# Performance work log

Measured on AMD Instinct MI355X. Metric: run time of the kernel, lower is better.

Reference implementation:

```python
import jax, jax.numpy as jnp
import numpy as np

H, W = 256, 256
N = H * W
C0, C1, C2 = 16, 32, 64  # base, base*2, base*4


def _grid_edges(h, w):
    """8-neighborhood grid edges (directed, both directions) + self loops."""
    idx = np.arange(h * w).reshape(h, w)
    srcs, dsts = [], []
    for dy in (-1, 0, 1):
        for dx in (-1, 0, 1):
            if dy == 0 and dx == 0:
                continue
            s = idx[max(0, -dy):h - max(0, dy), max(0, -dx):w - max(0, dx)]
            d = idx[max(0, dy):h - max(0, -dy), max(0, dx):w - max(0, -dx)]
            srcs.append(s.ravel()); dsts.append(d.ravel())
    srcs.append(np.arange(h * w)); dsts.append(np.arange(h * w))  # GATConv add_self_loops
    return np.concatenate(srcs).astype(np.int32), np.concatenate(dsts).astype(np.int32)


def _conv2d(x, w, b, pad):
    y = jax.lax.conv_general_dilated(x, w, (1, 1), [(pad, pad), (pad, pad)],
                                     dimension_numbers=('NCHW', 'OIHW', 'NCHW'))
    return y + b[None, :, None, None]


def _bn(x, g, b, eps=1e-5):
    # training-mode BatchNorm2d: biased batch statistics over (N,H,W)
    mu = x.mean((0, 2, 3), keepdims=True)
    var = ((x - mu) ** 2).mean((0, 2, 3), keepdims=True)
    return g[None, :, None, None] * (x - mu) * jax.lax.rsqrt(var + eps) + b[None, :, None, None]


def _gat(xg, w, a_s, a_d, b, src, dst):
    # PyG GATConv, heads=1: gather -> leaky_relu attention -> softmax over dst -> scatter-add
    def one(xn):
        h = xn @ w.T                                   # [N, C_out]
        e = jax.nn.leaky_relu((h @ a_s)[src] + (h @ a_d)[dst], 0.2)  # [E]
        m = jax.ops.segment_max(e, dst, num_segments=N)
        p = jnp.exp(e - m[dst])
        denom = jax.ops.segment_sum(p, dst, num_segments=N)
        agg = jax.ops.segment_sum(h[src] * p[:, None], dst, num_segments=N)
        return agg / (denom[:, None] + 1e-16) + b
    return jax.vmap(one)(xg)


def _gcb(x, pos_w, pos_b, gw, gas, gad, gb, src, dst):
    B, C = x.shape[0], x.shape[1]
    px = jnp.linspace(-1.0, 1.0, W)
    py = jnp.linspace(-1.0, 1.0, H)
    gx, gy = jnp.meshgrid(px, py, indexing='xy')       # each (H, W)
    pos = jnp.stack([gy, gx], -1)                      # (H, W, 2)
    pe = pos @ pos_w.T + pos_b                         # (H, W, C)
    x = x + pe.transpose(2, 0, 1)[None]
    xg = x.transpose(0, 2, 3, 1).reshape(B, N, C)      # batch of disjoint graphs -> vmap
    out = _gat(xg, gw, gas, gad, gb, src, dst)
    return out.reshape(B, H, W, -1).transpose(0, 3, 1, 2)


def _forward(x, conv1_w, conv1_b, bn1_g, bn1_b,
             pos1_w, pos1_b, gat1_w, gat1_as, gat1_ad, gat1_b, bn2_g, bn2_b,
             pos2_w, pos2_b, gat2_w, gat2_as, gat2_ad, gat2_b, bn3_g, bn3_b,
             mlp1_w, mlp1_b, mlp2_w, mlp2_b, filt, filt_bias,
             enh1_w, enh1_b, enh2_w, enh2_b, bn4_g, bn4_b, src, dst):
    f = _bn(jax.nn.relu(_conv2d(x, conv1_w, conv1_b, 2)), bn1_g, bn1_b)
    f = _bn(jax.nn.relu(_gcb(f, pos1_w, pos1_b, gat1_w, gat1_as, gat1_ad, gat1_b, src, dst)), bn2_g, bn2_b)
    f = _bn(jax.nn.relu(_gcb(f, pos2_w, pos2_b, gat2_w, gat2_as, gat2_ad, gat2_b, src, dst)), bn3_g, bn3_b)
    pooled = f.mean((2, 3))                            # AdaptiveAvgPool2d(1)
    h = jax.nn.relu(pooled @ mlp1_w.T + mlp1_b)
    cw = jax.nn.softmax(h @ mlp2_w.T + mlp2_b, axis=1)[:, :, None, None]
    wf = f * cw
    ff = wf * filt + filt_bias
    enh = _conv2d(jax.nn.relu(_conv2d(ff, enh1_w, enh1_b, 1)), enh2_w, enh2_b, 1) + ff
    return _bn(jax.nn.relu(enh), bn4_g, bn4_b)


def setup_inputs() -> dict:
    key = jax.random.key(0)
    ks = iter(jax.random.split(key, 40))
    def rn(shape, s=0.1):
        return jax.random.normal(next(ks), shape, dtype=jnp.float32) * s
    src, dst = _grid_edges(H, W)
    return {
        'x': jax.random.normal(next(ks), (2, 1, H, W), dtype=jnp.float32),
        'conv1_w': rn((C0, 1, 5, 5)), 'conv1_b': rn((C0,)),
        'bn1_g': jnp.ones((C0,)), 'bn1_b': jnp.zeros((C0,)),
        'pos1_w': rn((C0, 2)), 'pos1_b': rn((C0,)),
        'gat1_w': rn((C1, C0)), 'gat1_as': rn((C1,)), 'gat1_ad': rn((C1,)), 'gat1_b': rn((C1,)),
        'bn2_g': jnp.ones((C1,)), 'bn2_b': jnp.zeros((C1,)),
        'pos2_w': rn((C1, 2)), 'pos2_b': rn((C1,)),
        'gat2_w': rn((C2, C1)), 'gat2_as': rn((C2,)), 'gat2_ad': rn((C2,)), 'gat2_b': rn((C2,)),
        'bn3_g': jnp.ones((C2,)), 'bn3_b': jnp.zeros((C2,)),
        'mlp1_w': rn((C2 // 4, C2)), 'mlp1_b': rn((C2 // 4,)),
        'mlp2_w': rn((C2, C2 // 4)), 'mlp2_b': rn((C2,)),
        'filt': jnp.ones((1, C2, H, W)), 'filt_bias': jnp.zeros((1, C2, 1, 1)),
        'enh1_w': rn((C2 // 2, C2, 3, 3)), 'enh1_b': rn((C2 // 2,)),
        'enh2_w': rn((C2, C2 // 2, 3, 3)), 'enh2_b': rn((C2,)),
        'bn4_g': jnp.ones((C2,)), 'bn4_b': jnp.zeros((C2,)),
        'src': jnp.asarray(src), 'dst': jnp.asarray(dst),
    }


def reference(x, conv1_w, conv1_b, bn1_g, bn1_b,
              pos1_w, pos1_b, gat1_w, gat1_as, gat1_ad, gat1_b, bn2_g, bn2_b,
              pos2_w, pos2_b, gat2_w, gat2_as, gat2_ad, gat2_b, bn3_g, bn3_b,
              mlp1_w, mlp1_b, mlp2_w, mlp2_b, filt, filt_bias,
              enh1_w, enh1_b, enh2_w, enh2_b, bn4_g, bn4_b, src, dst):
    return _forward(x, conv1_w, conv1_b, bn1_g, bn1_b,
                    pos1_w, pos1_b, gat1_w, gat1_as, gat1_ad, gat1_b, bn2_g, bn2_b,
                    pos2_w, pos2_b, gat2_w, gat2_as, gat2_ad, gat2_b, bn3_g, bn3_b,
                    mlp1_w, mlp1_b, mlp2_w, mlp2_b, filt, filt_bias,
                    enh1_w, enh1_b, enh2_w, enh2_b, bn4_g, bn4_b, src, dst)
```

## Files before the change

### kernel.cpp

```cpp
#include <hip/hip_runtime.h>
#include <math.h>

#define HH 256
#define WW 256
#define NPIX 65536
#define BATCH 2

#define OFF_W0   0u
#define OFF_W1   8388608u
#define OFF_W2   16777216u
#define OFF_W3   20971520u
#define OFF_S    25165824u
#define OFF_D    25296896u
#define OFF_STAT 25427968u
#define OFF_ST1  (OFF_STAT + 0u)
#define OFF_ST2  (OFF_STAT + 64u)
#define OFF_ST3  (OFF_STAT + 192u)
#define OFF_ST4  (OFF_STAT + 448u)
#define OFF_CW   (OFF_STAT + 576u)
#define STAT_ZERO_N 704
#define OFF_WB1  (OFF_STAT + 704u)
#define OFF_WB2  (OFF_WB1 + 18432u)

typedef __attribute__((ext_vector_type(8))) short bf8v;
typedef __attribute__((ext_vector_type(4))) float f4v;
typedef __attribute__((ext_vector_type(4))) unsigned short us4;

#define GLL16(g, l) __builtin_amdgcn_global_load_lds(                               \
    (const __attribute__((address_space(1))) unsigned int*)(g),                    \
    (__attribute__((address_space(3))) unsigned int*)(l), 16, 0, 0)

__device__ __forceinline__ unsigned short f2bf(float f) {
    unsigned u = __float_as_uint(f);
    return (unsigned short)((u + 0x7FFFu + ((u >> 16) & 1u)) >> 16);
}
__device__ __forceinline__ float bf2f(unsigned short u) {
    return __uint_as_float(((unsigned)u) << 16);
}

__device__ __forceinline__ void bn_coef(const float* __restrict__ raw,
                                        const float* __restrict__ g,
                                        const float* __restrict__ b,
                                        int C, int c, float& A, float& Bv) {
    const float inv = 1.f / (float)(BATCH * NPIX);
    float mu  = raw[c] * inv;
    float var = raw[C + c] * inv - mu * mu;
    float rinv = rsqrtf(var + 1e-5f);
    A  = g[c] * rinv;
    Bv = b[c] - A * mu;
}

__device__ __forceinline__ void wave_red2(float& s, float& q) {
#pragma unroll
    for (int off = 32; off; off >>= 1) {
        s += __shfl_xor(s, off);
        q += __shfl_xor(q, off);
    }
}

__device__ __forceinline__ void row_swz512(int bid, int& y, int& b) {
    int orig = (bid & 7) * 64 + (bid >> 3);
    y = orig & 255;
    b = orig >> 8;
}

__global__ void prep(float* __restrict__ st,
                     const float* __restrict__ w1, unsigned short* __restrict__ wb1,
                     const float* __restrict__ w2, unsigned short* __restrict__ wb2) {
    int bid = blockIdx.x, tid = threadIdx.x;
    if (bid < 3) {
        int i = bid * 256 + tid;
        if (i < STAT_ZERO_N) st[i] = 0.f;
    } else if (bid < 75) {
        int i = (bid - 3) * 256 + tid;
        int co = i / (64 * 9);
        int rem = i - co * 64 * 9;
        int ci = rem / 9;
        int pos = rem - ci * 9;
        wb1[(pos * 32 + co) * 64 + ci] = f2bf(w1[i]);
    } else {
        int i = (bid - 75) * 256 + tid;
        int co = i / (32 * 9);
        int rem = i - co * 32 * 9;
        int ci = rem / 9;
        int pos = rem - ci * 9;
        wb2[(pos * 64 + co) * 32 + ci] = f2bf(w2[i]);
    }
}

__global__ __launch_bounds__(256) void conv5x5_all(const float* __restrict__ x,
                                                   const float* __restrict__ w,
                                                   const float* __restrict__ bias,
                                                   unsigned short* __restrict__ out,
                                                   float* __restrict__ st) {
    int y = blockIdx.x, b = blockIdx.y;
    int xx = threadIdx.x;
    __shared__ float lds[5 * 260];
    __shared__ float red[2][16][4];
    for (int i = threadIdx.x; i < 5 * 260; i += 256) {
        int r = i / 260, pos = i - r * 260;
        int yy = y + r - 2, xc = pos - 2;
        float v = 0.f;
        if ((unsigned)yy < 256u && (unsigned)xc < 256u) v = x[(b << 16) + (yy << 8) + xc];
        lds[i] = v;
    }
    __syncthreads();
    float v[25];
#pragma unroll
    for (int r = 0; r < 5; r++)
#pragma unroll
        for (int c = 0; c < 5; c++) v[r * 5 + c] = lds[r * 260 + xx + c];
    int lane = threadIdx.x & 63, wv = threadIdx.x >> 6;
#pragma unroll
    for (int co = 0; co < 16; co++) {
        float acc = bias[co];
#pragma unroll
        for (int k = 0; k < 25; k++) acc = fmaf(v[k], w[co * 25 + k], acc);
        acc = fmaxf(acc, 0.f);
        out[((size_t)(b * 16 + co) << 16) + (y << 8) + xx] = f2bf(acc);
        float s = acc, q = acc * acc;
        wave_red2(s, q);
        if (lane == 0) { red[0][co][wv] = s; red[1][co][wv] = q; }
    }
    __syncthreads();
    if (threadIdx.x < 16) {
        int co = threadIdx.x;
        float s = red[0][co][0] + red[0][co][1] + red[0][co][2] + red[0][co][3];
        float q = red[1][co][0] + red[1][co][1] + red[1][co][2] + red[1][co][3];
        atomicAdd(&st[co], s);
        atomicAdd(&st[16 + co], q);
    }
}

template <int CI, int CO>
__global__ void gat_pre(const unsigned short* __restrict__ f, const float* __restrict__ raw,
                        const float* __restrict__ bng, const float* __restrict__ bnb,
                        const float* __restrict__ posw, const float* __restrict__ posb,
                        const float* __restrict__ gw, const float* __restrict__ gas,
                        const float* __restrict__ gad,
                        unsigned short* __restrict__ hout, float* __restrict__ sout,
                        float* __restrict__ dout) {
    int tid = blockIdx.x * 256 + threadIdx.x;
    int n = tid & (NPIX - 1);
    int b = tid >> 16;
    int y = n >> 8, x = n & 255;
    float py = y * (2.f / 255.f) - 1.f;
    float px = x * (2.f / 255.f) - 1.f;
    float v[CI];
#pragma unroll
    for (int ci = 0; ci < CI; ci++) {
        float A, Bv;
        bn_coef(raw, bng, bnb, CI, ci, A, Bv);
        float t = fmaf(bf2f(f[(size_t)(b * CI + ci) * NPIX + n]), A, Bv);
        v[ci] = t + posw[2 * ci] * py + posw[2 * ci + 1] * px + posb[ci];
    }
    float s = 0.f, d = 0.f;
    for (int co = 0; co < CO; co++) {
        float acc = 0.f;
#pragma unroll
        for (int ci = 0; ci < CI; ci++) acc = fmaf(v[ci], gw[co * CI + ci], acc);
        hout[(size_t)(b * CO + co) * NPIX + n] = f2bf(acc);
        s = fmaf(acc, gas[co], s);
        d = fmaf(acc, gad[co], d);
    }
    sout[tid] = s;
    dout[tid] = d;
}

template <int CO, bool POOL>
__global__ __launch_bounds__(256) void gat_stencil_mfma(const unsigned short* __restrict__ hb,
                                                        const float* __restrict__ sbuf,
                                                        const float* __restrict__ dbuf,
                                                        const float* __restrict__ gb,
                                                        unsigned short* __restrict__ out,
                                                        float* __restrict__ st) {
    constexpr int NT2 = CO / 32;
    constexpr int CH = CO / 2;
    int bid = blockIdx.x;
    int orig = (bid & 7) * 128 + (bid >> 3);
    int coh = orig & 1;
    int rowu = orig >> 1;
    int y = rowu & 255;
    int b = rowu >> 8;
    int tid = threadIdx.x, lane = tid & 63, wid = tid >> 6;
    int m = lane & 15, grp = lane >> 4;
    int xw = wid * 64;
    int x = xw + lane;
    float di = dbuf[(b << 16) + (y << 8) + x];
    float p[9], mx = -1e30f;
#pragma unroll
    for (int k = 0; k < 9; k++) {
        int dy = k / 3 - 1, dx = k % 3 - 1;
        int yy = y + dy, xxn = x + dx;
        bool ok = ((unsigned)yy < 256u) && ((unsigned)xxn < 256u);
        float e = -1e30f;
        if (ok) {
            float t = sbuf[(b << 16) + (yy << 8) + xxn] + di;
            e = t > 0.f ? t : 0.2f * t;
        }
        p[k] = e;
        mx = fmaxf(mx, e);
    }
    float den = 0.f;
#pragma unroll
    for (int k = 0; k < 9; k++) { p[k] = __expf(p[k] - mx); den += p[k]; }
    float rden = 1.f / (den + 1e-16f);
    unsigned short pb[9];
#pragma unroll
    for (int k = 0; k < 9; k++) pb[k] = f2bf(p[k] * rden);
    unsigned pk0 = (unsigned)pb[0] | ((unsigned)pb[1] << 16);
    unsigned pk1 = (unsigned)pb[2] | ((unsigned)pb[3] << 16);
    unsigned pk2 = (unsigned)pb[4] | ((unsigned)pb[5] << 16);
    unsigned pk3 = (unsigned)pb[6] | ((unsigned)pb[7] << 16);
    unsigned pk4 = (unsigned)pb[8];
    float sAcc[NT2], qAcc[NT2], bb[NT2];
#pragma unroll
    for (int ct = 0; ct < NT2; ct++) {
        sAcc[ct] = 0.f; qAcc[ct] = 0.f;
        bb[ct] = gb[coh * CH + ct * 16 + m];
    }
#pragma unroll 1
    for (int t = 0; t < 4; t++) {
        int xb = xw + t * 16;
        int src = t * 16 + m;
        unsigned rk0 = __shfl(pk0, src);
        unsigned rk1 = __shfl(pk1, src);
        unsigned rk2 = __shfl(pk2, src);
        unsigned rk3 = __shfl(pk3, src);
        unsigned rk4 = __shfl(pk4, src);
        unsigned short rb[9];
        rb[0] = (unsigned short)rk0; rb[1] = (unsigned short)(rk0 >> 16);
        rb[2] = (unsigned short)rk1; rb[3] = (unsigned short)(rk1 >> 16);
        rb[4] = (unsigned short)rk2; rb[5] = (unsigned short)(rk2 >> 16);
        rb[6] = (unsigned short)rk3; rb[7] = (unsigned short)(rk3 >> 16);
        rb[8] = (unsigned short)rk4;
        union { bf8v v; unsigned short h[8]; } af[3];
#pragma unroll
        for (int dyi = 0; dyi < 3; dyi++)
#pragma unroll
            for (int j = 0; j < 8; j++) {
                int k = grp * 8 + j;
                int d = k - 8 - m;
                af[dyi].h[j] = (d >= -1 && d <= 1) ? rb[dyi * 3 + d + 1] : (unsigned short)0;
            }
        f4v acc[NT2];
        f4v z4 = {0.f, 0.f, 0.f, 0.f};
#pragma unroll
        for (int ct = 0; ct < NT2; ct++) acc[ct] = z4;
        int px0 = xb - 8 + grp * 8;
        px0 = px0 < 0 ? 0 : (px0 > 248 ? 248 : px0);
#pragma unroll
        for (int dyi = 0; dyi < 3; dyi++) {
            int yy = y + dyi - 1;
            if ((unsigned)yy >= 256u) continue;
#pragma unroll
            for (int ct = 0; ct < NT2; ct++) {
                int ch = coh * CH + ct * 16 + m;
                bf8v bv = *(const bf8v*)(hb + (((size_t)(b * CO + ch)) << 16) + (yy << 8) + px0);
                acc[ct] = __builtin_amdgcn_mfma_f32_16x16x32_bf16(af[dyi].v, bv, acc[ct], 0, 0, 0);
            }
        }
        int pxr = xb + grp * 4;
#pragma unroll
        for (int ct = 0; ct < NT2; ct++) {
            int ch = coh * CH + ct * 16 + m;
            f4v a = acc[ct];
            float o0 = fmaxf(a[0] + bb[ct], 0.f);
            float o1 = fmaxf(a[1] + bb[ct], 0.f);
            float o2 = fmaxf(a[2] + bb[ct], 0.f);
            float o3 = fmaxf(a[3] + bb[ct], 0.f);
            us4 pkst = {f2bf(o0), f2bf(o1), f2bf(o2), f2bf(o3)};
            *(us4*)(out + (((size_t)(b * CO + ch)) << 16) + (y << 8) + pxr) = pkst;
            sAcc[ct] += o0 + o1 + o2 + o3;
            qAcc[ct] += o0 * o0 + o1 * o1 + o2 * o2 + o3 * o3;
        }
    }
#pragma unroll
    for (int ct = 0; ct < NT2; ct++) {
        sAcc[ct] += __shfl_xor(sAcc[ct], 16); sAcc[ct] += __shfl_xor(sAcc[ct], 32);
        qAcc[ct] += __shfl_xor(qAcc[ct], 16); qAcc[ct] += __shfl_xor(qAcc[ct], 32);
    }
    __shared__ float red[2][NT2][16][4];
    if (grp == 0) {
#pragma unroll
        for (int ct = 0; ct < NT2; ct++) {
            red[0][ct][m][wid] = sAcc[ct];
            red[1][ct][m][wid] = qAcc[ct];
        }
    }
    __syncthreads();
    if (tid < CH) {
        int ct = tid >> 4, mm = tid & 15;
        int c = coh * CH + tid;
        float s = red[0][ct][mm][0] + red[0][ct][mm][1] + red[0][ct][mm][2] + red[0][ct][mm][3];
        float qq = red[1][ct][mm][0] + red[1][ct][mm][1] + red[1][ct][mm][2] + red[1][ct][mm][3];
        atomicAdd(&st[c], s);
        atomicAdd(&st[CO + c], qq);
        if (POOL) atomicAdd(&st[2 * CO + b * CO + c], s);
    }
}

__global__ void mlp_cw(const float* __restrict__ raw3, const float* __restrict__ g3,
                       const float* __restrict__ b3, const float* __restrict__ w1,
                       const float* __restrict__ bb1, const float* __restrict__ w2,
                       const float* __restrict__ bb2, float* __restrict__ cw) {
    __shared__ float pooled[2][64];
    __shared__ float hsh[2][16];
    int tid = threadIdx.x;
    {
        int b = tid >> 6, c = tid & 63;
        float A, Bv;
        bn_coef(raw3, g3, b3, 64, c, A, Bv);
        float sm = raw3[128 + (b << 6) + c];
        pooled[b][c] = fmaf(sm * (1.f / 65536.f), A, Bv);
    }
    __syncthreads();
    if (tid < 32) {
        int b = tid >> 4, j = tid & 15;
        float acc = bb1[j];
        for (int c2 = 0; c2 < 64; c2++) acc = fmaf(pooled[b][c2], w1[(j << 6) + c2], acc);
        hsh[b][j] = fmaxf(acc, 0.f);
    }
    __syncthreads();
    int b = tid >> 6, c = tid & 63;
    float logit = bb2[c];
    for (int j = 0; j < 16; j++) logit = fmaf(hsh[b][j], w2[(c << 4) + j], logit);
    float mm = logit;
#pragma unroll
    for (int off = 32; off; off >>= 1) mm = fmaxf(mm, __shfl_xor(mm, off));
    float e = __expf(logit - mm);
    float ss = e;
#pragma unroll
    for (int off = 32; off; off >>= 1) ss += __shfl_xor(ss, off);
    cw[(b << 6) + c] = e / ss;
}

__global__ __launch_bounds__(256) void ff_t(const unsigned short* __restrict__ g64,
                                            const float* __restrict__ raw3,
                                            const float* __restrict__ g3,
                                            const float* __restrict__ b3,
                                            const float* __restrict__ cw,
                                            const float* __restrict__ filt,
                                            const float* __restrict__ fbias,
                                            unsigned short* __restrict__ ffout,
                                            unsigned* __restrict__ at1) {
    int pxb = blockIdx.x * 64;
    int b = pxb >> 16;
    int nb = pxb & 65535;
    __shared__ unsigned t[64 * 33];
    int tid = threadIdx.x;
#pragma unroll
    for (int k = 0; k < 2; k++) {
        int u = tid + k * 256;
        int q = u & 15;
        int cp = u >> 4;
        int ch0 = cp * 2, ch1 = ch0 + 1;
        float A0, B0, A1, B1;
        bn_coef(raw3, g3, b3, 64, ch0, A0, B0);
        bn_coef(raw3, g3, b3, 64, ch1, A1, B1);
        float s0 = cw[(b << 6) + ch0], s1 = cw[(b << 6) + ch1];
        float fb0 = fbias[ch0], fb1 = fbias[ch1];
        int n = nb + q * 4;
        us4 r0 = *(const us4*)(g64 + ((size_t)(b * 64 + ch0) << 16) + n);
        us4 r1 = *(const us4*)(g64 + ((size_t)(b * 64 + ch1) << 16) + n);
        float4 l0 = *(const float4*)(filt + ((size_t)ch0 << 16) + n);
        float4 l1 = *(const float4*)(filt + ((size_t)ch1 << 16) + n);
        float4 o0, o1;
        o0.x = fmaf(fmaf(bf2f(r0[0]), A0, B0) * s0, l0.x, fb0);
        o0.y = fmaf(fmaf(bf2f(r0[1]), A0, B0) * s0, l0.y, fb0);
        o0.z = fmaf(fmaf(bf2f(r0[2]), A0, B0) * s0, l0.z, fb0);
        o0.w = fmaf(fmaf(bf2f(r0[3]), A0, B0) * s0, l0.w, fb0);
        o1.x = fmaf(fmaf(bf2f(r1[0]), A1, B1) * s1, l1.x, fb1);
        o1.y = fmaf(fmaf(bf2f(r1[1]), A1, B1) * s1, l1.y, fb1);
        o1.z = fmaf(fmaf(bf2f(r1[2]), A1, B1) * s1, l1.z, fb1);
        o1.w = fmaf(fmaf(bf2f(r1[3]), A1, B1) * s1, l1.w, fb1);
        us4 f0 = {f2bf(o0.x), f2bf(o0.y), f2bf(o0.z), f2bf(o0.w)};
        us4 f1 = {f2bf(o1.x), f2bf(o1.y), f2bf(o1.z), f2bf(o1.w)};
        *(us4*)(ffout + ((size_t)(b * 64 + ch0) << 16) + n) = f0;
        *(us4*)(ffout + ((size_t)(b * 64 + ch1) << 16) + n) = f1;
#pragma unroll
        for (int i = 0; i < 4; i++)
            t[(q * 4 + i) * 33 + cp] = (unsigned)f0[i] | ((unsigned)f1[i] << 16);
    }
    __syncthreads();
#pragma unroll
    for (int j = 0; j < 8; j++) {
        int lin = j * 256 + tid;
        int pl = lin >> 5, cp = lin & 31;
        unsigned v = t[pl * 33 + cp];
        int P = pxb + pl;
        size_t byte = ((size_t)P << 7) + ((cp >= 16) ? 64 : 0)
                    + (((cp & 15) * 4) ^ (((P >> 1) & 3) << 4));
        *(unsigned*)((char*)at1 + byte) = v;
    }
}

__global__ __launch_bounds__(256) void enh1_mfma(const unsigned short* __restrict__ at1,
                                                 const unsigned short* __restrict__ wb,
                                                 const float* __restrict__ bias,
                                                 unsigned short* __restrict__ at2) {
    int y, b;
    row_swz512(blockIdx.x, y, b);
    int tid = threadIdx.x;
    int lane = tid & 63, wid = tid >> 6;
    __shared__ __align__(16) unsigned short lds_u16[3 * 258 * 32];
    char* ldsb = (char*)lds_u16;
    {
        bf8v z = {0, 0, 0, 0, 0, 0, 0, 0};
        for (int i = tid; i < 3 * 258 * 32 / 8; i += 256) ((bf8v*)lds_u16)[i] = z;
    }
    f4v acc[4][2];
    {
        f4v z4 = {0.f, 0.f, 0.f, 0.f};
#pragma unroll
        for (int m = 0; m < 4; m++) { acc[m][0] = z4; acc[m][1] = z4; }
    }
#pragma unroll 1
    for (int kh = 0; kh < 2; kh++) {
        __syncthreads();
        for (int c = wid; c < 48; c += 4) {
            int r = c >> 4, k = c & 15;
            int yy = y + r - 1;
            if ((unsigned)yy < 256u) {
                const char* src = (const char*)at1
                    + (((size_t)((b << 16) + (yy << 8)) + (k * 16 + (lane >> 2))) << 7)
                    + kh * 64 + (lane & 3) * 16;
                char* dst = ldsb + (r * 258 + 1) * 64 + k * 1024;
                GLL16(src, dst);
            }
        }
        __syncthreads();
        bf8v bw0[9], bw1[9];
#pragma unroll
        for (int pos = 0; pos < 9; pos++) {
            bw0[pos] = *(const bf8v*)(wb + (pos * 32 + (lane & 15)) * 64 + kh * 32 + (lane >> 4) * 8);
            bw1[pos] = *(const bf8v*)(wb + (pos * 32 + 16 + (lane & 15)) * 64 + kh * 32 + (lane >> 4) * 8);
        }
#pragma unroll
        for (int mt = 0; mt < 4; mt++) {
            int xb = (wid * 4 + mt) * 16 + (lane & 15);
#pragma unroll
            for (int ky = 0; ky < 3; ky++) {
#pragma unroll
                for (int kx = 0; kx < 3; kx++) {
                    int x = xb + kx - 1;
                    int s = x + 1;
                    int off = (ky * 258 + s) * 64 + (((lane >> 4) * 16) ^ (((x >> 1) & 3) << 4));
                    bf8v a = *(const bf8v*)(ldsb + off);
                    acc[mt][0] = __builtin_amdgcn_mfma_f32_16x16x32_bf16(a, bw0[ky * 3 + kx], acc[mt][0], 0, 0, 0);
                    acc[mt][1] = __builtin_amdgcn_mfma_f32_16x16x32_bf16(a, bw1[ky * 3 + kx], acc[mt][1], 0, 0, 0);
                }
            }
        }
    }
    float bb[2] = {bias[lane & 15], bias[16 + (lane & 15)]};
#pragma unroll
    for (int mt = 0; mt < 4; mt++) {
#pragma unroll
        for (int nt = 0; nt < 2; nt++) {
            f4v v = acc[mt][nt];
            int co = nt * 16 + (lane & 15);
#pragma unroll
            for (int r = 0; r < 4; r++) {
                int x = (wid * 4 + mt) * 16 + (lane >> 4) * 4 + r;
                float val = fmaxf(v[r] + bb[nt], 0.f);
                size_t byte = (((size_t)((b << 16) + (y << 8) + x)) << 6)
                            + ((co * 2) ^ (((x >> 1) & 3) << 4));
                *(unsigned short*)((char*)at2 + byte) = f2bf(val);
            }
        }
    }
}

__global__ __launch_bounds__(256) void enh2_mfma(const unsigned short* __restrict__ at2,
                                                 const unsigned short* __restrict__ wb,
                                                 const float* __restrict__ bias,
                                                 const unsigned short* __restrict__ ff,
                                                 float* __restrict__ out,
                                                 float* __restrict__ st) {
    int y, b;
    row_swz512(blockIdx.x, y, b);
    int tid = threadIdx.x;
    int lane = tid & 63, wid = tid >> 6;
    __shared__ __align__(16) unsigned short lds_u16[3 * 258 * 32];
    char* ldsb = (char*)lds_u16;
    {
        bf8v z = {0, 0, 0, 0, 0, 0, 0, 0};
        for (int i = tid; i < 3 * 258 * 32 / 8; i += 256) ((bf8v*)lds_u16)[i] = z;
    }
    __syncthreads();
    for (int c = wid; c < 48; c += 4) {
        int r = c >> 4, k = c & 15;
        int yy = y + r - 1;
        if ((unsigned)yy < 256u) {
            const char* src = (const char*)at2
                + (((size_t)((b << 16) + (yy << 8))) << 6) + k * 1024 + lane * 16;
            char* dst = ldsb + (r * 258 + 1) * 64 + k * 1024;
            GLL16(src, dst);
        }
    }
    __syncthreads();
    f4v acc[4][4];
    {
        f4v z4 = {0.f, 0.f, 0.f, 0.f};
#pragma unroll
        for (int m = 0; m < 4; m++)
#pragma unroll
            for (int n = 0; n < 4; n++) acc[m][n] = z4;
    }
#pragma unroll
    for (int np = 0; np < 2; np++) {
        bf8v bw0[9], bw1[9];
#pragma unroll
        for (int pos = 0; pos < 9; pos++) {
            bw0[pos] = *(const bf8v*)(wb + (pos * 64 + np * 32 + (lane & 15)) * 32 + (lane >> 4) * 8);
            bw1[pos] = *(const bf8v*)(wb + (pos * 64 + np * 32 + 16 + (lane & 15)) * 32 + (lane >> 4) * 8);
        }
#pragma unroll
        for (int mt = 0; mt < 4; mt++) {
            int xb = (wid * 4 + mt) * 16 + (lane & 15);
#pragma unroll
            for (int ky = 0; ky < 3; ky++) {
#pragma unroll
                for (int kx = 0; kx < 3; kx++) {
                    int x = xb + kx - 1;
                    int s = x + 1;
                    int off = (ky * 258 + s) * 64 + (((lane >> 4) * 16) ^ (((x >> 1) & 3) << 4));
                    bf8v a = *(const bf8v*)(ldsb + off);
                    acc[mt][2 * np]     = __builtin_amdgcn_mfma_f32_16x16x32_bf16(a, bw0[ky * 3 + kx], acc[mt][2 * np], 0, 0, 0);
                    acc[mt][2 * np + 1] = __builtin_amdgcn_mfma_f32_16x16x32_bf16(a, bw1[ky * 3 + kx], acc[mt][2 * np + 1], 0, 0, 0);
                }
            }
        }
    }
    __syncthreads();
    float* red = (float*)lds_u16;
#pragma unroll
    for (int nt = 0; nt < 4; nt++) {
        int co = nt * 16 + (lane & 15);
        float bb = bias[co];
        float s = 0.f, q = 0.f;
#pragma unroll
        for (int mt = 0; mt < 4; mt++) {
            int xb4 = (wid * 4 + mt) * 16 + (lane >> 4) * 4;
            size_t idx = ((size_t)(b * 64 + co) << 16) + (y << 8) + xb4;
            us4 rv = *(const us4*)(ff + idx);
            f4v a = acc[mt][nt];
            float4 o;
            o.x = fmaxf(a[0] + bb + bf2f(rv[0]), 0.f);
            o.y = fmaxf(a[1] + bb + bf2f(rv[1]), 0.f);
            o.z = fmaxf(a[2] + bb + bf2f(rv[2]), 0.f);
            o.w = fmaxf(a[3] + bb + bf2f(rv[3]), 0.f);
            *(float4*)(out + idx) = o;
            s += o.x + o.y + o.z + o.w;
            q += o.x * o.x + o.y * o.y + o.z * o.z + o.w * o.w;
        }
        s += __shfl_xor(s, 16); s += __shfl_xor(s, 32);
        q += __shfl_xor(q, 16); q += __shfl_xor(q, 32);
        if (lane < 16) {
            red[(co * 4 + wid) * 2 + 0] = s;
            red[(co * 4 + wid) * 2 + 1] = q;
        }
    }
    __syncthreads();
    if (tid < 64) {
        float s = 0.f, q = 0.f;
#pragma unroll
        for (int w = 0; w < 4; w++) {
            s += red[(tid * 4 + w) * 2 + 0];
            q += red[(tid * 4 + w) * 2 + 1];
        }
        atomicAdd(&st[tid], s);
        atomicAdd(&st[64 + tid], q);
    }
}

__global__ void bn_apply4(float4* __restrict__ io, const float* __restrict__ raw,
                          const float* __restrict__ g, const float* __restrict__ b) {
    int t = blockIdx.x * 256 + threadIdx.x;
    int c = (t >> 14) & 63;
    float A, Bv;
    bn_coef(raw, g, b, 64, c, A, Bv);
    float4 v = io[t];
    v.x = fmaf(v.x, A, Bv);
    v.y = fmaf(v.y, A, Bv);
    v.z = fmaf(v.z, A, Bv);
    v.w = fmaf(v.w, A, Bv);
    io[t] = v;
}

extern "C" void kernel_launch(void* const* d_in, const int* in_sizes, int n_in,
                              void* d_out, int out_size, void* d_ws, size_t ws_size,
                              hipStream_t stream) {
    const float* x       = (const float*)d_in[0];
    const float* conv1_w = (const float*)d_in[1];
    const float* conv1_b = (const float*)d_in[2];
    const float* bn1_g   = (const float*)d_in[3];
    const float* bn1_b   = (const float*)d_in[4];
    const float* pos1_w  = (const float*)d_in[5];
    const float* pos1_b  = (const float*)d_in[6];
    const float* gat1_w  = (const float*)d_in[7];
    const float* gat1_as = (const float*)d_in[8];
    const float* gat1_ad = (const float*)d_in[9];
    const float* gat1_b  = (const float*)d_in[10];
    const float* bn2_g   = (const float*)d_in[11];
    const float* bn2_b   = (const float*)d_in[12];
    const float* pos2_w  = (const float*)d_in[13];
    const float* pos2_b  = (const float*)d_in[14];
    const float* gat2_w  = (const float*)d_in[15];
    const float* gat2_as = (const float*)d_in[16];
    const float* gat2_ad = (const float*)d_in[17];
    const float* gat2_b  = (const float*)d_in[18];
    const float* bn3_g   = (const float*)d_in[19];
    const float* bn3_b   = (const float*)d_in[20];
    const float* mlp1_w  = (const float*)d_in[21];
    const float* mlp1_b  = (const float*)d_in[22];
    const float* mlp2_w  = (const float*)d_in[23];
    const float* mlp2_b  = (const float*)d_in[24];
    const float* filt    = (const float*)d_in[25];
    const float* fbias   = (const float*)d_in[26];
    const float* enh1_w  = (const float*)d_in[27];
    const float* enh1_b  = (const float*)d_in[28];
    const float* enh2_w  = (const float*)d_in[29];
    const float* enh2_b  = (const float*)d_in[30];
    const float* bn4_g   = (const float*)d_in[31];
    const float* bn4_b   = (const float*)d_in[32];

    float* ws = (float*)d_ws;
    unsigned short* P0 = (unsigned short*)(ws + OFF_W0);
    unsigned short* HB = (unsigned short*)(ws + OFF_W1);
    unsigned short* FFB = (unsigned short*)(ws + OFF_W1);
    unsigned* AT1 = (unsigned*)(ws + OFF_W2);
    unsigned short* AT2 = (unsigned short*)(ws + OFF_W3);
    float* SB = ws + OFF_S;
    float* DB = ws + OFF_D;
    float* ST1 = ws + OFF_ST1;
    float* ST2 = ws + OFF_ST2;
    float* ST3 = ws + OFF_ST3;
    float* ST4 = ws + OFF_ST4;
    float* CW  = ws + OFF_CW;
    unsigned short* WB1 = (unsigned short*)(ws + OFF_WB1);
    unsigned short* WB2 = (unsigned short*)(ws + OFF_WB2);
    float* out = (float*)d_out;

    prep<<<147, 256, 0, stream>>>(ws + OFF_STAT, enh1_w, WB1, enh2_w, WB2);

    conv5x5_all<<<dim3(256, 2), 256, 0, stream>>>(x, conv1_w, conv1_b, P0, ST1);

    gat_pre<16, 32><<<512, 256, 0, stream>>>(P0, ST1, bn1_g, bn1_b, pos1_w, pos1_b,
                                             gat1_w, gat1_as, gat1_ad, HB, SB, DB);

    gat_stencil_mfma<32, false><<<1024, 256, 0, stream>>>(HB, SB, DB, gat1_b, P0, ST2);

    gat_pre<32, 64><<<512, 256, 0, stream>>>(P0, ST2, bn2_g, bn2_b, pos2_w, pos2_b,
                                             gat2_w, gat2_as, gat2_ad, HB, SB, DB);

    gat_stencil_mfma<64, true><<<1024, 256, 0, stream>>>(HB, SB, DB, gat2_b, P0, ST3);

    mlp_cw<<<1, 128, 0, stream>>>(ST3, bn3_g, bn3_b, mlp1_w, mlp1_b, mlp2_w, mlp2_b, CW);

    ff_t<<<2048, 256, 0, stream>>>(P0, ST3, bn3_g, bn3_b, CW, filt, fbias, FFB, AT1);

    enh1_mfma<<<512, 256, 0, stream>>>((const unsigned short*)AT1, WB1, enh1_b, AT2);

    enh2_mfma<<<512, 256, 0, stream>>>(AT2, WB2, enh2_b, FFB, out, ST4);

    bn_apply4<<<32768 / 4, 256, 0, stream>>>((float4*)out, ST4, bn4_g, bn4_b);
}
```

Before: 189.4 us.

## Fuse channel-weight MLP into ff_t, stage enh2 output in bf16, hoist BN coefs

The single-block mlp_cw kernel is removed and every ff_t block now recomputes the pooled MLP and softmax channel weights into shared memory, saving a launch and a serialization point at the cost of redundant per-block work. enh2 now writes its pre-BN result as bf16 to a workspace buffer instead of fp32 to the output, and bn_apply4 reads the bf16 data and writes fp32, which cuts the intermediate read/write traffic but loses precision before normalization. gat_pre computes BN coefficients once per block in shared memory instead of per thread per channel.

```diff
diff --git a/kernel.cpp b/kernel.cpp
--- a/kernel.cpp
+++ b/kernel.cpp
@@ -17,7 +17,6 @@
 #define OFF_ST2  (OFF_STAT + 64u)
 #define OFF_ST3  (OFF_STAT + 192u)
 #define OFF_ST4  (OFF_STAT + 448u)
-#define OFF_CW   (OFF_STAT + 576u)
 #define STAT_ZERO_N 704
 #define OFF_WB1  (OFF_STAT + 704u)
 #define OFF_WB2  (OFF_WB1 + 18432u)
@@ -133,13 +132,22 @@
 }
 
 template <int CI, int CO>
-__global__ void gat_pre(const unsigned short* __restrict__ f, const float* __restrict__ raw,
+__global__ __launch_bounds__(256) void gat_pre(const unsigned short* __restrict__ f,
+                        const float* __restrict__ raw,
                         const float* __restrict__ bng, const float* __restrict__ bnb,
                         const float* __restrict__ posw, const float* __restrict__ posb,
                         const float* __restrict__ gw, const float* __restrict__ gas,
                         const float* __restrict__ gad,
                         unsigned short* __restrict__ hout, float* __restrict__ sout,
                         float* __restrict__ dout) {
+    __shared__ float Ash[CI], Bsh[CI];
+    if (threadIdx.x < CI) {
+        float A, Bv;
+        bn_coef(raw, bng, bnb, CI, threadIdx.x, A, Bv);
+        Ash[threadIdx.x] = A;
+        Bsh[threadIdx.x] = Bv + posb[threadIdx.x];
+    }
+    __syncthreads();
     int tid = blockIdx.x * 256 + threadIdx.x;
     int n = tid & (NPIX - 1);
     int b = tid >> 16;
@@ -149,10 +157,8 @@
     float v[CI];
 #pragma unroll
     for (int ci = 0; ci < CI; ci++) {
-        float A, Bv;
-        bn_coef(raw, bng, bnb, CI, ci, A, Bv);
-        float t = fmaf(bf2f(f[(size_t)(b * CI + ci) * NPIX + n]), A, Bv);
-        v[ci] = t + posw[2 * ci] * py + posw[2 * ci + 1] * px + posb[ci];
+        float t = fmaf(bf2f(f[(size_t)(b * CI + ci) * NPIX + n]), Ash[ci], Bsh[ci]);
+        v[ci] = t + posw[2 * ci] * py + posw[2 * ci + 1] * px;
     }
     float s = 0.f, d = 0.f;
     for (int co = 0; co < CO; co++) {
@@ -300,14 +306,24 @@
     }
 }
 
-__global__ void mlp_cw(const float* __restrict__ raw3, const float* __restrict__ g3,
-                       const float* __restrict__ b3, const float* __restrict__ w1,
-                       const float* __restrict__ bb1, const float* __restrict__ w2,
-                       const float* __restrict__ bb2, float* __restrict__ cw) {
+__global__ __launch_bounds__(256) void ff_t(const unsigned short* __restrict__ g64,
+                                            const float* __restrict__ raw3,
+                                            const float* __restrict__ g3,
+                                            const float* __restrict__ b3,
+                                            const float* __restrict__ w1,
+                                            const float* __restrict__ bb1,
+                                            const float* __restrict__ w2,
+                                            const float* __restrict__ bb2,
+                                            const float* __restrict__ filt,
+                                            const float* __restrict__ fbias,
+                                            unsigned short* __restrict__ ffout,
+                                            unsigned* __restrict__ at1) {
     __shared__ float pooled[2][64];
     __shared__ float hsh[2][16];
+    __shared__ float cwsh[2][64];
+    __shared__ unsigned t[64 * 33];
     int tid = threadIdx.x;
-    {
+    if (tid < 128) {
         int b = tid >> 6, c = tid & 63;
         float A, Bv;
         bn_coef(raw3, g3, b3, 64, c, A, Bv);
@@ -322,33 +338,23 @@
         hsh[b][j] = fmaxf(acc, 0.f);
     }
     __syncthreads();
-    int b = tid >> 6, c = tid & 63;
-    float logit = bb2[c];
-    for (int j = 0; j < 16; j++) logit = fmaf(hsh[b][j], w2[(c << 4) + j], logit);
-    float mm = logit;
-#pragma unroll
-    for (int off = 32; off; off >>= 1) mm = fmaxf(mm, __shfl_xor(mm, off));
-    float e = __expf(logit - mm);
-    float ss = e;
-#pragma unroll
-    for (int off = 32; off; off >>= 1) ss += __shfl_xor(ss, off);
-    cw[(b << 6) + c] = e / ss;
-}
-
-__global__ __launch_bounds__(256) void ff_t(const unsigned short* __restrict__ g64,
-                                            const float* __restrict__ raw3,
-                                            const float* __restrict__ g3,
-                                            const float* __restrict__ b3,
-                                            const float* __restrict__ cw,
-                                            const float* __restrict__ filt,
-                                            const float* __restrict__ fbias,
-                                            unsigned short* __restrict__ ffout,
-                                            unsigned* __restrict__ at1) {
+    if (tid < 128) {
+        int b = tid >> 6, c = tid & 63;
+        float logit = bb2[c];
+        for (int j = 0; j < 16; j++) logit = fmaf(hsh[b][j], w2[(c << 4) + j], logit);
+        float mm = logit;
+#pragma unroll
+        for (int off = 32; off; off >>= 1) mm = fmaxf(mm, __shfl_xor(mm, off));
+        float e = __expf(logit - mm);
+        float ss = e;
+#pragma unroll
+        for (int off = 32; off; off >>= 1) ss += __shfl_xor(ss, off);
+        cwsh[b][c] = e / ss;
+    }
+    __syncthreads();
     int pxb = blockIdx.x * 64;
     int b = pxb >> 16;
     int nb = pxb & 65535;
-    __shared__ unsigned t[64 * 33];
-    int tid = threadIdx.x;
 #pragma unroll
     for (int k = 0; k < 2; k++) {
         int u = tid + k * 256;
@@ -358,7 +364,7 @@
         float A0, B0, A1, B1;
         bn_coef(raw3, g3, b3, 64, ch0, A0, B0);
         bn_coef(raw3, g3, b3, 64, ch1, A1, B1);
-        float s0 = cw[(b << 6) + ch0], s1 = cw[(b << 6) + ch1];
+        float s0 = cwsh[b][ch0], s1 = cwsh[b][ch1];
         float fb0 = fbias[ch0], fb1 = fbias[ch1];
         int n = nb + q * 4;
         us4 r0 = *(const us4*)(g64 + ((size_t)(b * 64 + ch0) << 16) + n);
@@ -476,7 +482,7 @@
                                                  const unsigned short* __restrict__ wb,
                                                  const float* __restrict__ bias,
                                                  const unsigned short* __restrict__ ff,
-                                                 float* __restrict__ out,
+                                                 unsigned short* __restrict__ enh,
                                                  float* __restrict__ st) {
     int y, b;
     row_swz512(blockIdx.x, y, b);
@@ -546,14 +552,15 @@
             size_t idx = ((size_t)(b * 64 + co) << 16) + (y << 8) + xb4;
             us4 rv = *(const us4*)(ff + idx);
             f4v a = acc[mt][nt];
-            float4 o;
-            o.x = fmaxf(a[0] + bb + bf2f(rv[0]), 0.f);
-            o.y = fmaxf(a[1] + bb + bf2f(rv[1]), 0.f);
-            o.z = fmaxf(a[2] + bb + bf2f(rv[2]), 0.f);
-            o.w = fmaxf(a[3] + bb + bf2f(rv[3]), 0.f);
-            *(float4*)(out + idx) = o;
-            s += o.x + o.y + o.z + o.w;
-            q += o.x * o.x + o.y * o.y + o.z * o.z + o.w * o.w;
+            us4 ro;
+            ro[0] = f2bf(fmaxf(a[0] + bb + bf2f(rv[0]), 0.f));
+            ro[1] = f2bf(fmaxf(a[1] + bb + bf2f(rv[1]), 0.f));
+            ro[2] = f2bf(fmaxf(a[2] + bb + bf2f(rv[2]), 0.f));
+            ro[3] = f2bf(fmaxf(a[3] + bb + bf2f(rv[3]), 0.f));
+            *(us4*)(enh + idx) = ro;
+            float r0 = bf2f(ro[0]), r1 = bf2f(ro[1]), r2 = bf2f(ro[2]), r3 = bf2f(ro[3]);
+            s += r0 + r1 + r2 + r3;
+            q += r0 * r0 + r1 * r1 + r2 * r2 + r3 * r3;
         }
         s += __shfl_xor(s, 16); s += __shfl_xor(s, 32);
         q += __shfl_xor(q, 16); q += __shfl_xor(q, 32);
@@ -575,18 +582,20 @@
     }
 }
 
-__global__ void bn_apply4(float4* __restrict__ io, const float* __restrict__ raw,
+__global__ void bn_apply4(const us4* __restrict__ enh, float4* __restrict__ io,
+                          const float* __restrict__ raw,
                           const float* __restrict__ g, const float* __restrict__ b) {
     int t = blockIdx.x * 256 + threadIdx.x;
     int c = (t >> 14) & 63;
     float A, Bv;
     bn_coef(raw, g, b, 64, c, A, Bv);
-    float4 v = io[t];
-    v.x = fmaf(v.x, A, Bv);
-    v.y = fmaf(v.y, A, Bv);
-    v.z = fmaf(v.z, A, Bv);
-    v.w = fmaf(v.w, A, Bv);
-    io[t] = v;
+    us4 v = enh[t];
+    float4 o;
+    o.x = fmaf(bf2f(v[0]), A, Bv);
+    o.y = fmaf(bf2f(v[1]), A, Bv);
+    o.z = fmaf(bf2f(v[2]), A, Bv);
+    o.w = fmaf(bf2f(v[3]), A, Bv);
+    io[t] = o;
 }
 
 extern "C" void kernel_launch(void* const* d_in, const int* in_sizes, int n_in,
@@ -631,6 +640,7 @@
     unsigned short* HB = (unsigned short*)(ws + OFF_W1);
     unsigned short* FFB = (unsigned short*)(ws + OFF_W1);
     unsigned* AT1 = (unsigned*)(ws + OFF_W2);
+    unsigned short* ENH = (unsigned short*)(ws + OFF_W2);
     unsigned short* AT2 = (unsigned short*)(ws + OFF_W3);
     float* SB = ws + OFF_S;
     float* DB = ws + OFF_D;
@@ -638,7 +648,6 @@
     float* ST2 = ws + OFF_ST2;
     float* ST3 = ws + OFF_ST3;
     float* ST4 = ws + OFF_ST4;
-    float* CW  = ws + OFF_CW;
     unsigned short* WB1 = (unsigned short*)(ws + OFF_WB1);
     unsigned short* WB2 = (unsigned short*)(ws + OFF_WB2);
     float* out = (float*)d_out;
@@ -657,13 +666,12 @@
 
     gat_stencil_mfma<64, true><<<1024, 256, 0, stream>>>(HB, SB, DB, gat2_b, P0, ST3);
 
-    mlp_cw<<<1, 128, 0, stream>>>(ST3, bn3_g, bn3_b, mlp1_w, mlp1_b, mlp2_w, mlp2_b, CW);
-
-    ff_t<<<2048, 256, 0, stream>>>(P0, ST3, bn3_g, bn3_b, CW, filt, fbias, FFB, AT1);
+    ff_t<<<2048, 256, 0, stream>>>(P0, ST3, bn3_g, bn3_b, mlp1_w, mlp1_b, mlp2_w, mlp2_b,
+                                   filt, fbias, FFB, AT1);
 
     enh1_mfma<<<512, 256, 0, stream>>>((const unsigned short*)AT1, WB1, enh1_b, AT2);
 
-    enh2_mfma<<<512, 256, 0, stream>>>(AT2, WB2, enh2_b, FFB, out, ST4);
-
-    bn_apply4<<<32768 / 4, 256, 0, stream>>>((float4*)out, ST4, bn4_g, bn4_b);
-}
+    enh2_mfma<<<512, 256, 0, stream>>>(AT2, WB2, enh2_b, FFB, ENH, ST4);
+
+    bn_apply4<<<8192, 256, 0, stream>>>((const us4*)ENH, (float4*)out, ST4, bn4_g, bn4_b);
+}
```

After: 185.5 us. 2.1% less time.
